# Optimization experiments

Measured on AMD Instinct MI355X. Metric: run time of the kernel, lower is better.

## Reference

```python
import jax, jax.numpy as jnp
import numpy as np

B, T, E = 2, 2048, 2048
H, D = 16, 128
KVH = H // 2
THETA = 10000.0

def make_rope(dim, seq_len, theta):
    inv_freqs = 1.0 / (theta ** (jnp.arange(0, dim, 2, dtype=jnp.float32) / dim))
    positions = jnp.arange(seq_len, dtype=jnp.float32)
    freqs = positions[:, None] * inv_freqs[None, :]  # (T, D/2)
    return jax.lax.complex(jnp.cos(freqs), jnp.sin(freqs))

def apply_rope(x, rope):
    # x: (B, h, T, D), rope: (T, D/2) complex
    xr = x.astype(jnp.float32).reshape(*x.shape[:-1], -1, 2)
    xc = jax.lax.complex(xr[..., 0], xr[..., 1])
    out = xc * rope[None, None, :, :]
    return jnp.stack([jnp.real(out), jnp.imag(out)], axis=-1).reshape(x.shape).astype(x.dtype)

def setup_inputs() -> dict:
    key = jax.random.key(0)
    ks = jax.random.split(key, 5)
    x = jax.random.normal(ks[0], (B, T, E), dtype=jnp.float32)
    mask = jnp.tril(jnp.ones((T, T), dtype=jnp.int32))[None, None]  # causal (1,1,T,T)
    s = 0.02
    wq = jax.random.normal(ks[1], (E, H * D), dtype=jnp.float32) * s
    wk = jax.random.normal(ks[2], (E, KVH * D), dtype=jnp.float32) * s
    wv = jax.random.normal(ks[3], (E, KVH * D), dtype=jnp.float32) * s
    wo = jax.random.normal(ks[4], (H * D, E), dtype=jnp.float32) * s
    return {"x": x, "mask": mask, "wq": wq, "wk": wk, "wv": wv, "wo": wo}

def reference(x, mask, wq, wk, wv, wo):
    rope = make_rope(D, T, THETA)
    q = (x @ wq).reshape(B, T, H, D).transpose(0, 2, 1, 3)      # (B,H,T,D)
    k = (x @ wk).reshape(B, T, KVH, D).transpose(0, 2, 1, 3)    # (B,KVH,T,D)
    v = (x @ wv).reshape(B, T, KVH, D).transpose(0, 2, 1, 3)
    q = apply_rope(q, rope)
    k = apply_rope(k, rope)
    # GQA: repeat kv heads to match query heads
    k = jnp.repeat(k, H // KVH, axis=1)
    v = jnp.repeat(v, H // KVH, axis=1)
    scale = D ** -0.5
    attn = jnp.einsum('bhqd,bhkd->bhqk', q, k) * scale
    attn = jnp.where(mask == 0, -jnp.inf, attn)
    attn = jax.nn.softmax(attn, axis=-1)
    attn = jnp.where(jnp.isnan(attn), 0.0, attn)
    out = jnp.einsum('bhqk,bhkd->bhqd', attn, v)
    out = out.transpose(0, 2, 1, 3).reshape(B, T, H * D)
    return out @ wo
```

## Files before the change

kernel.cpp:

```cpp
#include <hip/hip_runtime.h>
#include <math.h>

#define Bb   2
#define Tt   2048
#define Ee   2048
#define Hh   16
#define KVHh 8
#define Dd   128
#define Mm   (Bb*Tt)

typedef unsigned short u16;
typedef __bf16 bf16x8 __attribute__((ext_vector_type(8)));
typedef float  f32x4  __attribute__((ext_vector_type(4)));

__device__ __forceinline__ u16 f2b(float f) {
    union { float f; unsigned u; } v; v.f = f;
    unsigned r = v.u + 0x7fffu + ((v.u >> 16) & 1u);
    return (u16)(r >> 16);
}
__device__ __forceinline__ u16 f2b_fast(float f) {
    union { float f; unsigned u; } v; v.f = f;
    return (u16)((v.u + 0x8000u) >> 16);
}
__device__ __forceinline__ float b2f(u16 h) {
    union { float f; unsigned u; } v; v.u = ((unsigned)h) << 16;
    return v.f;
}

__device__ __forceinline__ void gl_lds16(const u16* g, u16* l) {
    __builtin_amdgcn_global_load_lds(
        (const __attribute__((address_space(1))) void*)g,
        (__attribute__((address_space(3))) void*)l,
        16, 0, 0);
}

__global__ void cast_x_kernel(const float* __restrict__ x, u16* __restrict__ xb, int n4) {
    int i = blockIdx.x * blockDim.x + threadIdx.x;
    if (i >= n4) return;
    float4 f = ((const float4*)x)[i];
    unsigned lo = (unsigned)f2b(f.x) | ((unsigned)f2b(f.y) << 16);
    unsigned hi = (unsigned)f2b(f.z) | ((unsigned)f2b(f.w) << 16);
    ((uint2*)xb)[i] = make_uint2(lo, hi);
}

__global__ void transpose_cast4_kernel(const float* __restrict__ wq, const float* __restrict__ wk,
                                       const float* __restrict__ wv, const float* __restrict__ wo,
                                       u16* __restrict__ btqkv, u16* __restrict__ bto) {
    __shared__ float tile[32][33];
    int job = blockIdx.z;
    const float* W; u16* Bt; int C;
    if (job == 0)      { W = wq; Bt = btqkv;                      C = 2048; }
    else if (job == 1) { W = wk; Bt = btqkv + (size_t)2048 * Ee;  C = 1024; }
    else if (job == 2) { W = wv; Bt = btqkv + (size_t)3072 * Ee;  C = 1024; }
    else               { W = wo; Bt = bto;                        C = 2048; }
    int c0 = blockIdx.x * 32, r0 = blockIdx.y * 32;
    if (c0 >= C) return;
    int x = threadIdx.x, y = threadIdx.y;
    for (int j = y; j < 32; j += 8)
        tile[j][x] = W[(size_t)(r0 + j) * C + c0 + x];
    __syncthreads();
    for (int j = y; j < 32; j += 8)
        Bt[(size_t)(c0 + j) * 2048 + r0 + x] = f2b(tile[x][j]);
}

__global__ void transpose_v_kernel(const u16* __restrict__ v, u16* __restrict__ vt) {
    __shared__ u16 tile[32][34];
    int x = threadIdx.x, y = threadIdx.y;
    int c0 = blockIdx.x * 32;
    int r0 = blockIdx.y * 32;
    int bk = blockIdx.z;
    for (int j = y; j < 32; j += 8)
        tile[j][x] = v[((size_t)bk * Tt + r0 + j) * Dd + c0 + x];
    __syncthreads();
    for (int j = y; j < 32; j += 8)
        vt[((size_t)bk * Dd + c0 + j) * Tt + r0 + x] = tile[x][j];
}

__global__ void rope_kernel(u16* __restrict__ q, u16* __restrict__ k) {
    const int QP = Bb * Hh * Tt * (Dd / 2);
    const int KP = Bb * KVHh * Tt * (Dd / 2);
    int idx = blockIdx.x * blockDim.x + threadIdx.x;
    if (idx >= QP + KP) return;
    u16* ptr; int p;
    if (idx < QP) { ptr = q; p = idx; } else { ptr = k; p = idx - QP; }
    int d2 = p & 63;
    int row = p >> 6;
    int t = row & (Tt - 1);
    float ex = (float)(2 * d2) * (1.0f / 128.0f);
    float inv = expf(-ex * 9.210340371976184f);
    float fr = (float)t * inv;
    float c = cosf(fr), s = sinf(fr);
    size_t e0 = (size_t)row * Dd + 2 * d2;
    unsigned pair = *(const unsigned*)(ptr + e0);
    float x0 = b2f((u16)(pair & 0xffff));
    float x1 = b2f((u16)(pair >> 16));
    float o0 = x0 * c - x1 * s;
    float o1 = x0 * s + x1 * c;
    *(unsigned*)(ptr + e0) = (unsigned)f2b(o0) | ((unsigned)f2b(o1) << 16);
}

__global__ __launch_bounds__(256) void gemm_kernel(
    const u16* __restrict__ A, const u16* __restrict__ Bt,
    int Mdim, int Ndim, int Kdim, int mode,
    u16* __restrict__ qo, u16* __restrict__ ko, u16* __restrict__ vo,
    float* __restrict__ fo)
{
    __shared__ u16 Ash[128 * 64];
    __shared__ u16 Bsh[128 * 64];
    int tid = threadIdx.x;
    int lane = tid & 63, wv = tid >> 6;
    int quad = lane >> 4, l15 = lane & 15;
    int bn = blockIdx.x, bm = blockIdx.y;
    int wm = (wv >> 1) * 64, wn = (wv & 1) * 64;
    const int rowA0 = bm * 128, rowB0 = bn * 128;
    int srow = lane >> 3;
    int scol = (lane & 7) * 8;

    f32x4 acc[4][4];
#pragma unroll
    for (int i = 0; i < 4; i++)
#pragma unroll
        for (int j = 0; j < 4; j++) acc[i][j] = (f32x4){0.f, 0.f, 0.f, 0.f};

    for (int kb = 0; kb < Kdim; kb += 64) {
#pragma unroll
        for (int j = 0; j < 4; j++) {
            int chunk = wv * 4 + j;
            int r = chunk * 8 + srow;
            gl_lds16(A  + (size_t)(rowA0 + r) * Kdim + kb + scol, Ash + chunk * 512);
            gl_lds16(Bt + (size_t)(rowB0 + r) * Kdim + kb + scol, Bsh + chunk * 512);
        }
        __syncthreads();
#pragma unroll
        for (int kc = 0; kc < 2; kc++) {
            bf16x8 af[4], bfr[4];
#pragma unroll
            for (int i = 0; i < 4; i++)
                af[i] = *(const bf16x8*)(Ash + (wm + i * 16 + l15) * 64 + kc * 32 + quad * 8);
#pragma unroll
            for (int i = 0; i < 4; i++)
                bfr[i] = *(const bf16x8*)(Bsh + (wn + i * 16 + l15) * 64 + kc * 32 + quad * 8);
#pragma unroll
            for (int i = 0; i < 4; i++)
#pragma unroll
                for (int j = 0; j < 4; j++)
                    acc[i][j] = __builtin_amdgcn_mfma_f32_16x16x32_bf16(af[i], bfr[j], acc[i][j], 0, 0, 0);
        }
        __syncthreads();
    }

#pragma unroll
    for (int i = 0; i < 4; i++)
#pragma unroll
        for (int j = 0; j < 4; j++)
#pragma unroll
            for (int r = 0; r < 4; r++) {
                int m = rowA0 + wm + i * 16 + quad * 4 + r;
                int n = rowB0 + wn + j * 16 + l15;
                float val = acc[i][j][r];
                if (mode == 0) {
                    int b = m >> 11, t = m & (Tt - 1);
                    if (n < 2048) {
                        int h = n >> 7, d = n & 127;
                        qo[(((size_t)(b * Hh + h)) * Tt + t) * Dd + d] = f2b(val);
                    } else if (n < 3072) {
                        int h = (n - 2048) >> 7, d = n & 127;
                        ko[(((size_t)(b * KVHh + h)) * Tt + t) * Dd + d] = f2b(val);
                    } else {
                        int h = (n - 3072) >> 7, d = n & 127;
                        vo[(((size_t)(b * KVHh + h)) * Tt + t) * Dd + d] = f2b(val);
                    }
                } else {
                    fo[(size_t)m * Ndim + n] = val;
                }
            }
}

#define LDKV 136
#define LDVT 72
#define LDP  72

__global__ __launch_bounds__(256) void flash_kernel(
    const u16* __restrict__ q, const u16* __restrict__ k, const u16* __restrict__ vt,
    u16* __restrict__ attn)
{
    __shared__ u16 Ksh[64 * LDKV];
    __shared__ u16 Vtsh[128 * LDVT];
    __shared__ u16 Psh[128 * LDP];

    int tid = threadIdx.x, lane = tid & 63, w = tid >> 6;
    int quad = lane >> 4, l15 = lane & 15;
    int pr = blockIdx.x;
    int bh = blockIdx.y;
    int b = bh >> 4, h = bh & 15;
    int kvh = h >> 1;
    const u16* qbase = q + (size_t)bh * Tt * Dd;
    const u16* kbase = k + ((size_t)(b * KVHh + kvh)) * Tt * Dd;
    const u16* vtbase = vt + ((size_t)(b * KVHh + kvh)) * Dd * Tt;
    u16* P0 = Psh + (2 * w) * 16 * LDP;
    u16* P1 = Psh + (2 * w + 1) * 16 * LDP;
    const float sc2 = 0.08838834764831845f * 1.4426950408889634f;

    for (int half = 0; half < 2; half++) {
        int qt = half ? (15 - pr) : pr;
        int row0 = qt * 128 + w * 32;

        bf16x8 qf0[4], qf1[4];
        {
            const u16* qr0 = qbase + (size_t)(row0 + l15) * Dd + quad * 8;
            const u16* qr1 = qbase + (size_t)(row0 + 16 + l15) * Dd + quad * 8;
#pragma unroll
            for (int c = 0; c < 4; c++) {
                qf0[c] = *(const bf16x8*)(qr0 + c * 32);
                qf1[c] = *(const bf16x8*)(qr1 + c * 32);
            }
        }

        f32x4 o0[8], o1[8];
#pragma unroll
        for (int i = 0; i < 8; i++) { o0[i] = (f32x4){0.f,0.f,0.f,0.f}; o1[i] = (f32x4){0.f,0.f,0.f,0.f}; }
        float l0[4] = {0.f,0.f,0.f,0.f}, l1[4] = {0.f,0.f,0.f,0.f};

        int nkt = 2 * (qt + 1);
        for (int kt = 0; kt < nkt; kt++) {
#pragma unroll
            for (int j = 0; j < 4; j++) {
                int chunk = j * 256 + tid;
                int rk = chunk >> 4, ck = chunk & 15;
                uint4 dk = *(const uint4*)(kbase + (size_t)(kt * 64 + rk) * Dd + ck * 8);
                *(uint4*)(Ksh + rk * LDKV + ck * 8) = dk;
                int rv = chunk >> 3, cv = chunk & 7;
                uint4 dv = *(const uint4*)(vtbase + (size_t)rv * Tt + kt * 64 + cv * 8);
                *(uint4*)(Vtsh + rv * LDVT + cv * 8) = dv;
            }
            __syncthreads();

            bool skip = (kt * 64) > (row0 + 31);
            if (!skip) {
                f32x4 s0[4], s1[4];
#pragma unroll
                for (int ni = 0; ni < 4; ni++) { s0[ni] = (f32x4){0.f,0.f,0.f,0.f}; s1[ni] = (f32x4){0.f,0.f,0.f,0.f}; }
#pragma unroll
                for (int c = 0; c < 4; c++)
#pragma unroll
                    for (int ni = 0; ni < 4; ni++) {
                        bf16x8 kf = *(const bf16x8*)(Ksh + (ni * 16 + l15) * LDKV + c * 32 + quad * 8);
                        s0[ni] = __builtin_amdgcn_mfma_f32_16x16x32_bf16(qf0[c], kf, s0[ni], 0, 0, 0);
                        s1[ni] = __builtin_amdgcn_mfma_f32_16x16x32_bf16(qf1[c], kf, s1[ni], 0, 0, 0);
                    }

                if (kt * 64 + 63 > row0) {
#pragma unroll
                    for (int ni = 0; ni < 4; ni++)
#pragma unroll
                        for (int r = 0; r < 4; r++) {
                            int kcol = kt * 64 + ni * 16 + l15;
                            int qa = row0 + quad * 4 + r;
                            int qb2 = row0 + 16 + quad * 4 + r;
                            if (kcol > qa)  s0[ni][r] = -__builtin_inff();
                            if (kcol > qb2) s1[ni][r] = -__builtin_inff();
                        }
                }

#pragma unroll
                for (int ni = 0; ni < 4; ni++)
#pragma unroll
                    for (int r = 0; r < 4; r++) {
                        float p0 = exp2f(s0[ni][r] * sc2);
                        l0[r] += p0;
                        P0[(quad * 4 + r) * LDP + ni * 16 + l15] = f2b_fast(p0);
                        float p1 = exp2f(s1[ni][r] * sc2);
                        l1[r] += p1;
                        P1[(quad * 4 + r) * LDP + ni * 16 + l15] = f2b_fast(p1);
                    }
            }
            __syncthreads();

            if (!skip) {
#pragma unroll
                for (int c = 0; c < 2; c++) {
                    bf16x8 pf0 = *(const bf16x8*)(P0 + l15 * LDP + c * 32 + quad * 8);
                    bf16x8 pf1 = *(const bf16x8*)(P1 + l15 * LDP + c * 32 + quad * 8);
#pragma unroll
                    for (int di = 0; di < 8; di++) {
                        bf16x8 vf = *(const bf16x8*)(Vtsh + (di * 16 + l15) * LDVT + c * 32 + quad * 8);
                        o0[di] = __builtin_amdgcn_mfma_f32_16x16x32_bf16(pf0, vf, o0[di], 0, 0, 0);
                        o1[di] = __builtin_amdgcn_mfma_f32_16x16x32_bf16(pf1, vf, o1[di], 0, 0, 0);
                    }
                }
            }
            __syncthreads();
        }

        float linv0[4], linv1[4];
#pragma unroll
        for (int r = 0; r < 4; r++) {
            float a = l0[r];
            a += __shfl_xor(a, 1); a += __shfl_xor(a, 2);
            a += __shfl_xor(a, 4); a += __shfl_xor(a, 8);
            linv0[r] = 1.0f / a;
            float c2 = l1[r];
            c2 += __shfl_xor(c2, 1); c2 += __shfl_xor(c2, 2);
            c2 += __shfl_xor(c2, 4); c2 += __shfl_xor(c2, 8);
            linv1[r] = 1.0f / c2;
        }
#pragma unroll
        for (int di = 0; di < 8; di++)
#pragma unroll
            for (int r = 0; r < 4; r++) {
                int ta = row0 + quad * 4 + r;
                int tb = row0 + 16 + quad * 4 + r;
                size_t ma = (size_t)b * Tt + ta;
                size_t mb = (size_t)b * Tt + tb;
                attn[ma * (Hh * Dd) + h * Dd + di * 16 + l15] = f2b(o0[di][r] * linv0[r]);
                attn[mb * (Hh * Dd) + h * Dd + di * 16 + l15] = f2b(o1[di][r] * linv1[r]);
            }
        __syncthreads();
    }
}

extern "C" void kernel_launch(void* const* d_in, const int* in_sizes, int n_in,
                              void* d_out, int out_size, void* d_ws, size_t ws_size,
                              hipStream_t stream) {
    const float* x  = (const float*)d_in[0];
    const float* wq = (const float*)d_in[2];
    const float* wk = (const float*)d_in[3];
    const float* wv = (const float*)d_in[4];
    const float* wo = (const float*)d_in[5];
    float* out = (float*)d_out;

    char* ws = (char*)d_ws;
    u16* xb    = (u16*)ws; ws += (size_t)Mm * Ee * 2;
    u16* btqkv = (u16*)ws; ws += (size_t)4096 * Ee * 2;
    u16* bto   = (u16*)ws; ws += (size_t)Ee * (Hh * Dd) * 2;
    u16* qb    = (u16*)ws; ws += (size_t)Bb * Hh * Tt * Dd * 2;
    u16* kb    = (u16*)ws; ws += (size_t)Bb * KVHh * Tt * Dd * 2;
    u16* vb    = (u16*)ws; ws += (size_t)Bb * KVHh * Tt * Dd * 2;
    u16* vtb   = (u16*)ws; ws += (size_t)Bb * KVHh * Dd * Tt * 2;
    u16* attn  = (u16*)ws; ws += (size_t)Mm * (Hh * Dd) * 2;

    cast_x_kernel<<<(Mm * Ee / 4 + 255) / 256, 256, 0, stream>>>(x, xb, Mm * Ee / 4);

    transpose_cast4_kernel<<<dim3(64, 64, 4), dim3(32, 8), 0, stream>>>(wq, wk, wv, wo, btqkv, bto);

    gemm_kernel<<<dim3(32, 32), 256, 0, stream>>>(xb, btqkv, Mm, 4096, Ee, 0,
                                                  qb, kb, vb, nullptr);

    {
        int total = Bb * Hh * Tt * 64 + Bb * KVHh * Tt * 64;
        rope_kernel<<<(total + 255) / 256, 256, 0, stream>>>(qb, kb);
    }

    transpose_v_kernel<<<dim3(Dd / 32, Tt / 32, Bb * KVHh), dim3(32, 8), 0, stream>>>(vb, vtb);

    flash_kernel<<<dim3(Tt / 256, Bb * Hh), 256, 0, stream>>>(qb, kb, vtb, attn);

    gemm_kernel<<<dim3(16, 32), 256, 0, stream>>>(attn, bto, Mm, 2048, Hh * Dd, 1,
                                                  nullptr, nullptr, nullptr, out);
}
```

Measured before the change: 407.3 us.

## Merge prep kernels, prefetch K/V tiles into registers, hoist GEMM load pointers

The x cast is folded into the weight transpose-cast kernel, and rope is merged with the V transpose, which removes two kernel launches. In the flash kernel, the next K and Vt tiles are loaded from global memory into registers while the current tile is being computed, so load latency overlaps with the MFMA work. The GEMM precomputes its per-thread global load pointers and advances them each step instead of recomputing the addresses. The register prefetch raises register pressure in the flash kernel, which could lower occupancy.

```diff
diff --git a/kernel.cpp b/kernel.cpp
--- a/kernel.cpp
+++ b/kernel.cpp
@@ -34,20 +34,26 @@
         16, 0, 0);
 }
 
-__global__ void cast_x_kernel(const float* __restrict__ x, u16* __restrict__ xb, int n4) {
-    int i = blockIdx.x * blockDim.x + threadIdx.x;
-    if (i >= n4) return;
-    float4 f = ((const float4*)x)[i];
-    unsigned lo = (unsigned)f2b(f.x) | ((unsigned)f2b(f.y) << 16);
-    unsigned hi = (unsigned)f2b(f.z) | ((unsigned)f2b(f.w) << 16);
-    ((uint2*)xb)[i] = make_uint2(lo, hi);
-}
-
-__global__ void transpose_cast4_kernel(const float* __restrict__ wq, const float* __restrict__ wk,
-                                       const float* __restrict__ wv, const float* __restrict__ wo,
-                                       u16* __restrict__ btqkv, u16* __restrict__ bto) {
+__global__ void prep_kernel(const float* __restrict__ x, u16* __restrict__ xb,
+                            const float* __restrict__ wq, const float* __restrict__ wk,
+                            const float* __restrict__ wv, const float* __restrict__ wo,
+                            u16* __restrict__ btqkv, u16* __restrict__ bto) {
     __shared__ float tile[32][33];
     int job = blockIdx.z;
+    int tx = threadIdx.x, ty = threadIdx.y;
+    if (job == 4) {
+        int t = ty * 32 + tx;
+        int base = (blockIdx.y * 64 + blockIdx.x) * 512;
+#pragma unroll
+        for (int s = 0; s < 2; s++) {
+            int i = base + s * 256 + t;
+            float4 f = ((const float4*)x)[i];
+            unsigned lo = (unsigned)f2b(f.x) | ((unsigned)f2b(f.y) << 16);
+            unsigned hi = (unsigned)f2b(f.z) | ((unsigned)f2b(f.w) << 16);
+            ((uint2*)xb)[i] = make_uint2(lo, hi);
+        }
+        return;
+    }
     const float* W; u16* Bt; int C;
     if (job == 0)      { W = wq; Bt = btqkv;                      C = 2048; }
     else if (job == 1) { W = wk; Bt = btqkv + (size_t)2048 * Ee;  C = 1024; }
@@ -55,48 +61,48 @@
     else               { W = wo; Bt = bto;                        C = 2048; }
     int c0 = blockIdx.x * 32, r0 = blockIdx.y * 32;
     if (c0 >= C) return;
-    int x = threadIdx.x, y = threadIdx.y;
-    for (int j = y; j < 32; j += 8)
-        tile[j][x] = W[(size_t)(r0 + j) * C + c0 + x];
+    for (int j = ty; j < 32; j += 8)
+        tile[j][tx] = W[(size_t)(r0 + j) * C + c0 + tx];
     __syncthreads();
-    for (int j = y; j < 32; j += 8)
-        Bt[(size_t)(c0 + j) * 2048 + r0 + x] = f2b(tile[x][j]);
-}
-
-__global__ void transpose_v_kernel(const u16* __restrict__ v, u16* __restrict__ vt) {
+    for (int j = ty; j < 32; j += 8)
+        Bt[(size_t)(c0 + j) * 2048 + r0 + tx] = f2b(tile[tx][j]);
+}
+
+__global__ void rope_vt_kernel(u16* __restrict__ q, u16* __restrict__ k,
+                               const u16* __restrict__ v, u16* __restrict__ vt) {
     __shared__ u16 tile[32][34];
-    int x = threadIdx.x, y = threadIdx.y;
-    int c0 = blockIdx.x * 32;
-    int r0 = blockIdx.y * 32;
-    int bk = blockIdx.z;
+    int bx = blockIdx.x;
+    if (bx < 24576) {
+        const int QP = Bb * Hh * Tt * (Dd / 2);
+        int idx = bx * 256 + threadIdx.x;
+        u16* ptr; int p;
+        if (idx < QP) { ptr = q; p = idx; } else { ptr = k; p = idx - QP; }
+        int d2 = p & 63;
+        int row = p >> 6;
+        int t = row & (Tt - 1);
+        float ex = (float)(2 * d2) * (1.0f / 128.0f);
+        float inv = expf(-ex * 9.210340371976184f);
+        float fr = (float)t * inv;
+        float c = cosf(fr), s = sinf(fr);
+        size_t e0 = (size_t)row * Dd + 2 * d2;
+        unsigned pair = *(const unsigned*)(ptr + e0);
+        float x0 = b2f((u16)(pair & 0xffff));
+        float x1 = b2f((u16)(pair >> 16));
+        float o0 = x0 * c - x1 * s;
+        float o1 = x0 * s + x1 * c;
+        *(unsigned*)(ptr + e0) = (unsigned)f2b(o0) | ((unsigned)f2b(o1) << 16);
+        return;
+    }
+    int bx2 = bx - 24576;
+    int c0 = (bx2 & 3) * 32;
+    int r0 = ((bx2 >> 2) & 63) * 32;
+    int bk = bx2 >> 8;
+    int x = threadIdx.x & 31, y = threadIdx.x >> 5;
     for (int j = y; j < 32; j += 8)
         tile[j][x] = v[((size_t)bk * Tt + r0 + j) * Dd + c0 + x];
     __syncthreads();
     for (int j = y; j < 32; j += 8)
         vt[((size_t)bk * Dd + c0 + j) * Tt + r0 + x] = tile[x][j];
-}
-
-__global__ void rope_kernel(u16* __restrict__ q, u16* __restrict__ k) {
-    const int QP = Bb * Hh * Tt * (Dd / 2);
-    const int KP = Bb * KVHh * Tt * (Dd / 2);
-    int idx = blockIdx.x * blockDim.x + threadIdx.x;
-    if (idx >= QP + KP) return;
-    u16* ptr; int p;
-    if (idx < QP) { ptr = q; p = idx; } else { ptr = k; p = idx - QP; }
-    int d2 = p & 63;
-    int row = p >> 6;
-    int t = row & (Tt - 1);
-    float ex = (float)(2 * d2) * (1.0f / 128.0f);
-    float inv = expf(-ex * 9.210340371976184f);
-    float fr = (float)t * inv;
-    float c = cosf(fr), s = sinf(fr);
-    size_t e0 = (size_t)row * Dd + 2 * d2;
-    unsigned pair = *(const unsigned*)(ptr + e0);
-    float x0 = b2f((u16)(pair & 0xffff));
-    float x1 = b2f((u16)(pair >> 16));
-    float o0 = x0 * c - x1 * s;
-    float o1 = x0 * s + x1 * c;
-    *(unsigned*)(ptr + e0) = (unsigned)f2b(o0) | ((unsigned)f2b(o1) << 16);
 }
 
 __global__ __launch_bounds__(256) void gemm_kernel(
@@ -116,6 +122,14 @@
     int srow = lane >> 3;
     int scol = (lane & 7) * 8;
 
+    const u16* pa[4]; const u16* pb[4];
+#pragma unroll
+    for (int j = 0; j < 4; j++) {
+        int r = (wv * 4 + j) * 8 + srow;
+        pa[j] = A  + (size_t)(rowA0 + r) * Kdim + scol;
+        pb[j] = Bt + (size_t)(rowB0 + r) * Kdim + scol;
+    }
+
     f32x4 acc[4][4];
 #pragma unroll
     for (int i = 0; i < 4; i++)
@@ -126,9 +140,8 @@
 #pragma unroll
         for (int j = 0; j < 4; j++) {
             int chunk = wv * 4 + j;
-            int r = chunk * 8 + srow;
-            gl_lds16(A  + (size_t)(rowA0 + r) * Kdim + kb + scol, Ash + chunk * 512);
-            gl_lds16(Bt + (size_t)(rowB0 + r) * Kdim + kb + scol, Bsh + chunk * 512);
+            gl_lds16(pa[j], Ash + chunk * 512); pa[j] += 64;
+            gl_lds16(pb[j], Bsh + chunk * 512); pb[j] += 64;
         }
         __syncthreads();
 #pragma unroll
@@ -201,6 +214,9 @@
     u16* P1 = Psh + (2 * w + 1) * 16 * LDP;
     const float sc2 = 0.08838834764831845f * 1.4426950408889634f;
 
+    int krow = tid >> 4, kcol = (tid & 15) * 8;
+    int vrow = tid >> 3, vcol = (tid & 7) * 8;
+
     for (int half = 0; half < 2; half++) {
         int qt = half ? (15 - pr) : pr;
         int row0 = qt * 128 + w * 32;
@@ -221,19 +237,36 @@
         for (int i = 0; i < 8; i++) { o0[i] = (f32x4){0.f,0.f,0.f,0.f}; o1[i] = (f32x4){0.f,0.f,0.f,0.f}; }
         float l0[4] = {0.f,0.f,0.f,0.f}, l1[4] = {0.f,0.f,0.f,0.f};
 
+        const u16* pk[4]; const u16* pv[4];
+#pragma unroll
+        for (int j = 0; j < 4; j++) {
+            pk[j] = kbase + (size_t)(j * 16 + krow) * Dd + kcol;
+            pv[j] = vtbase + (size_t)(j * 32 + vrow) * Tt + vcol;
+        }
+
+        uint4 rK[4], rV[4];
+#pragma unroll
+        for (int j = 0; j < 4; j++) {
+            rK[j] = *(const uint4*)pk[j]; pk[j] += 64 * Dd;
+            rV[j] = *(const uint4*)pv[j]; pv[j] += 64;
+        }
+
         int nkt = 2 * (qt + 1);
         for (int kt = 0; kt < nkt; kt++) {
 #pragma unroll
             for (int j = 0; j < 4; j++) {
-                int chunk = j * 256 + tid;
-                int rk = chunk >> 4, ck = chunk & 15;
-                uint4 dk = *(const uint4*)(kbase + (size_t)(kt * 64 + rk) * Dd + ck * 8);
-                *(uint4*)(Ksh + rk * LDKV + ck * 8) = dk;
-                int rv = chunk >> 3, cv = chunk & 7;
-                uint4 dv = *(const uint4*)(vtbase + (size_t)rv * Tt + kt * 64 + cv * 8);
-                *(uint4*)(Vtsh + rv * LDVT + cv * 8) = dv;
+                *(uint4*)(Ksh + (j * 16 + krow) * LDKV + kcol) = rK[j];
+                *(uint4*)(Vtsh + (j * 32 + vrow) * LDVT + vcol) = rV[j];
             }
             __syncthreads();
+
+            if (kt + 1 < nkt) {
+#pragma unroll
+                for (int j = 0; j < 4; j++) {
+                    rK[j] = *(const uint4*)pk[j]; pk[j] += 64 * Dd;
+                    rV[j] = *(const uint4*)pv[j]; pv[j] += 64;
+                }
+            }
 
             bool skip = (kt * 64) > (row0 + 31);
             if (!skip) {
@@ -254,11 +287,11 @@
                     for (int ni = 0; ni < 4; ni++)
 #pragma unroll
                         for (int r = 0; r < 4; r++) {
-                            int kcol = kt * 64 + ni * 16 + l15;
+                            int kcol2 = kt * 64 + ni * 16 + l15;
                             int qa = row0 + quad * 4 + r;
                             int qb2 = row0 + 16 + quad * 4 + r;
-                            if (kcol > qa)  s0[ni][r] = -__builtin_inff();
-                            if (kcol > qb2) s1[ni][r] = -__builtin_inff();
+                            if (kcol2 > qa)  s0[ni][r] = -__builtin_inff();
+                            if (kcol2 > qb2) s1[ni][r] = -__builtin_inff();
                         }
                 }
 
@@ -339,19 +372,12 @@
     u16* vtb   = (u16*)ws; ws += (size_t)Bb * KVHh * Dd * Tt * 2;
     u16* attn  = (u16*)ws; ws += (size_t)Mm * (Hh * Dd) * 2;
 
-    cast_x_kernel<<<(Mm * Ee / 4 + 255) / 256, 256, 0, stream>>>(x, xb, Mm * Ee / 4);
-
-    transpose_cast4_kernel<<<dim3(64, 64, 4), dim3(32, 8), 0, stream>>>(wq, wk, wv, wo, btqkv, bto);
+    prep_kernel<<<dim3(64, 64, 5), dim3(32, 8), 0, stream>>>(x, xb, wq, wk, wv, wo, btqkv, bto);
 
     gemm_kernel<<<dim3(32, 32), 256, 0, stream>>>(xb, btqkv, Mm, 4096, Ee, 0,
                                                   qb, kb, vb, nullptr);
 
-    {
-        int total = Bb * Hh * Tt * 64 + Bb * KVHh * Tt * 64;
-        rope_kernel<<<(total + 255) / 256, 256, 0, stream>>>(qb, kb);
-    }
-
-    transpose_v_kernel<<<dim3(Dd / 32, Tt / 32, Bb * KVHh), dim3(32, 8), 0, stream>>>(vb, vtb);
+    rope_vt_kernel<<<24576 + 4096, 256, 0, stream>>>(qb, kb, vb, vtb);
 
     flash_kernel<<<dim3(Tt / 256, Bb * Hh), 256, 0, stream>>>(qb, kb, vtb, attn);
 
```

Measured after the change: 500.7 us. 22.9% more time.
